# Optimization experiments

Hardware: AMD Instinct MI355X
Metric: run time of the kernel (lower is better)

## Reference

```python
import jax, jax.numpy as jnp
import numpy as np

NUM_NODES = 1024
K = 16384
G = 128

def setup_inputs() -> dict:
    key = jax.random.key(0)
    k1, k2, k3 = jax.random.split(key, 3)
    x = jax.random.normal(k1, (G, NUM_NODES, 64), dtype=jnp.float32)
    # original draws fresh xavier-uniform embeddings inside forward; we
    # materialize equivalent random embeddings here (only ordering matters).
    emb_s = jax.random.normal(k2, (G, NUM_NODES, 1), dtype=jnp.float32)
    emb_t = jax.random.normal(k3, (G, 1, NUM_NODES), dtype=jnp.float32)
    return {"x": x, "emb_s": emb_s, "emb_t": emb_t}

def reference(x, emb_s, emb_t):
    num_graphs = x.shape[0]
    n = NUM_NODES
    # rank-1 outer product adjacency: [G, N, N]
    adj = emb_s * emb_t  # broadcast (G,N,1)*(G,1,N)
    # mask diagonal with -inf
    diag = jnp.eye(n, dtype=bool)
    adj = jnp.where(diag[None, :, :], -jnp.inf, adj)
    # global top-k over flattened N*N per graph
    adj_flat = adj.reshape(num_graphs, n * n)
    _, indices = jax.lax.top_k(adj_flat, K)  # [G, K]
    # scatter ones at selected positions
    out_flat = jnp.zeros((num_graphs, n * n), dtype=adj.dtype)
    rows = jnp.arange(num_graphs)[:, None]
    out_flat = out_flat.at[rows, indices].set(1.0)
    return out_flat.reshape(num_graphs, n, n)
```

## Files before the change

kernel.cpp:

```cpp
#include <hip/hip_runtime.h>
#include <stdint.h>

#define NNODES 1024
#define NGRAPH 128
#define TOPK   16384
#define EQCAP  4096
#define WROWS  8

typedef float vfloat4 __attribute__((ext_vector_type(4)));

__device__ __forceinline__ uint32_t fkey(float x) {
    uint32_t u = __float_as_uint(x);
    return (u & 0x80000000u) ? ~u : (u | 0x80000000u);
}
__device__ __forceinline__ float inv_fkey(uint32_t k) {
    uint32_t u = (k & 0x80000000u) ? (k & 0x7FFFFFFFu) : ~k;
    return __uint_as_float(u);
}

__global__ __launch_bounds__(NNODES)
void select_kernel(const float* __restrict__ s, const float* __restrict__ t,
                   uint32_t* __restrict__ Tout, uint32_t* __restrict__ Rout,
                   uint32_t* __restrict__ eqCntG, uint32_t* __restrict__ eqIdxG) {
    const int g = blockIdx.x, i = threadIdx.x;
    __shared__ uint64_t xbuf[2][NNODES];
    __shared__ float    tvs[NNODES];
    __shared__ uint16_t sidx[NNODES];
    __shared__ uint32_t wsum[16];
    __shared__ uint32_t sLo, sHi, sDir, sEqCnt;
    __shared__ uint32_t sEqList[EQCAP];

    const float tv_i = t[g * NNODES + i];
    uint64_t e = ((uint64_t)fkey(tv_i) << 16) | (uint32_t)i;
    if (i == 0) { sLo = 0u; sHi = 0xFFFFFFFFu; sEqCnt = 0u; }

    int pb = 0;
    for (int k = 2; k <= NNODES; k <<= 1) {
        for (int j = k >> 1; j > 0; j >>= 1) {
            uint64_t pe;
            if (j >= 64) {
                xbuf[pb][i] = e;
                __syncthreads();
                pe = xbuf[pb][i ^ j];
                pb ^= 1;
            } else {
                pe = (uint64_t)__shfl_xor((unsigned long long)e, j, 64);
            }
            bool keepSmall = (((i & j) == 0) == ((i & k) == 0));
            e = (keepSmall == (pe < e)) ? pe : e;
        }
    }
    tvs[i]  = inv_fkey((uint32_t)(e >> 16));
    sidx[i] = (uint16_t)(e & 0xFFFFu);

    const float sv = s[g * NNODES + i];
    const bool sneg = (__float_as_uint(sv) >> 31) != 0;
    const uint32_t kdiag = fkey(sv * tv_i);
    __syncthreads();

    auto srchRange = [&](uint32_t cand, int lo_, int hi_) -> int {
        while (lo_ < hi_) {
            int mid = (lo_ + hi_) >> 1;
            bool pred = fkey(sv * tvs[mid]) > cand;
            bool goLeft = sneg ? !pred : pred;
            if (goLeft) hi_ = mid; else lo_ = mid + 1;
        }
        return lo_;
    };

    int rlo = 0, rhi = NNODES;
    uint32_t cntHi = 0u;

    for (int it = 0; it < 33; ++it) {
        const uint32_t lo = sLo, hi = sHi;
        const uint32_t mid = lo + ((hi - lo) >> 1);
        const int b = srchRange(mid, rlo, rhi);
        uint32_t c = sneg ? (uint32_t)b : (uint32_t)(NNODES - b);
        if (kdiag > mid) c--;
        uint32_t r = c;
        for (int off = 32; off; off >>= 1) r += __shfl_down(r, off);
        if ((i & 63) == 0) wsum[i >> 6] = r;
        __syncthreads();
        if (i == 0 && lo < hi) {
            uint32_t tot = 0;
            for (int w = 0; w < 16; ++w) tot += wsum[w];
            if (tot < TOPK) { sHi = mid; sDir = 0u; cntHi = tot; }
            else            { sLo = mid + 1; sDir = 1u; }
        }
        __syncthreads();
        if (lo < hi) {
            if (sDir == 0u) { if (!sneg) rhi = b; else rlo = b; }
            else            { if (!sneg) rlo = b; else rhi = b; }
        }
    }
    const uint32_t T = sLo;
    if (i == 0) { Tout[g] = T; Rout[g] = TOPK - cntHi; }

    auto bound = [&](bool ge) -> int {
        int lo_ = 0, hi_ = NNODES;
        while (lo_ < hi_) {
            int mid = (lo_ + hi_) >> 1;
            uint32_t k = fkey(sv * tvs[mid]);
            bool pred = ge ? (k >= T) : (k > T);
            bool goLeft = sneg ? !pred : pred;
            if (goLeft) hi_ = mid; else lo_ = mid + 1;
        }
        return lo_;
    };
    int e0, e1;
    if (!sneg) { e0 = bound(true);  e1 = bound(false); }
    else       { e0 = bound(false); e1 = bound(true);  }
    for (int p = e0; p < e1; ++p) {
        uint32_t j = sidx[p];
        if ((int)j == i) continue;
        uint32_t slot = atomicAdd(&sEqCnt, 1u);
        if (slot < EQCAP) sEqList[slot] = (uint32_t)(i * NNODES) + j;
    }
    __syncthreads();
    uint32_t E = sEqCnt; if (E > EQCAP) E = EQCAP;
    if (i == 0) eqCntG[g] = E;
    for (uint32_t p = i; p < E; p += NNODES) eqIdxG[g * EQCAP + p] = sEqList[p];
}

__global__ __launch_bounds__(256)
void write_kernel(const float* __restrict__ s, const float* __restrict__ t,
                  const uint32_t* __restrict__ Tin, float* __restrict__ out) {
    const int b  = blockIdx.x;
    const int g  = b >> 7;
    const int i0 = (b & 127) * WROWS;
    const uint32_t T = Tin[g];
    const vfloat4 tv = ((const vfloat4*)(t + (size_t)g * NNODES))[threadIdx.x];
    const int j0 = threadIdx.x * 4;
    vfloat4* obase = (vfloat4*)(out + (size_t)g * NNODES * NNODES + (size_t)i0 * NNODES);
    #pragma unroll
    for (int r = 0; r < WROWS; ++r) {
        const int i = i0 + r;
        const float sv = s[(size_t)g * NNODES + i];
        vfloat4 o;
        o.x = (fkey(sv * tv.x) > T && (j0 + 0) != i) ? 1.0f : 0.0f;
        o.y = (fkey(sv * tv.y) > T && (j0 + 1) != i) ? 1.0f : 0.0f;
        o.z = (fkey(sv * tv.z) > T && (j0 + 2) != i) ? 1.0f : 0.0f;
        o.w = (fkey(sv * tv.w) > T && (j0 + 3) != i) ? 1.0f : 0.0f;
        __builtin_nontemporal_store(o, &obase[(size_t)r * (NNODES / 4) + threadIdx.x]);
    }
}

__global__ __launch_bounds__(256)
void scatter_kernel(const uint32_t* __restrict__ eqCnt, const uint32_t* __restrict__ eqIdx,
                    const uint32_t* __restrict__ Rin, float* __restrict__ out) {
    const int g = blockIdx.x;
    uint32_t E = eqCnt[g];
    const uint32_t R = Rin[g];
    __shared__ uint32_t se[EQCAP];
    for (uint32_t p = threadIdx.x; p < E; p += blockDim.x) se[p] = eqIdx[g * EQCAP + p];
    __syncthreads();
    for (uint32_t p = threadIdx.x; p < E; p += blockDim.x) {
        uint32_t v = se[p], rank = 0;
        for (uint32_t q = 0; q < E; ++q) rank += (se[q] < v) ? 1u : 0u;
        if (rank < R) out[(size_t)g * NNODES * NNODES + v] = 1.0f;
    }
}

extern "C" void kernel_launch(void* const* d_in, const int* in_sizes, int n_in,
                              void* d_out, int out_size, void* d_ws, size_t ws_size,
                              hipStream_t stream) {
    const float* s = (const float*)d_in[1];
    const float* t = (const float*)d_in[2];
    float* out = (float*)d_out;

    char* ws = (char*)d_ws;
    uint32_t* Tbuf  = (uint32_t*)ws; ws += (size_t)NGRAPH * 4;
    uint32_t* Rbuf  = (uint32_t*)ws; ws += (size_t)NGRAPH * 4;
    uint32_t* eqCnt = (uint32_t*)ws; ws += (size_t)NGRAPH * 4;
    uint32_t* eqIdx = (uint32_t*)ws; ws += (size_t)NGRAPH * EQCAP * 4;

    select_kernel<<<NGRAPH, NNODES, 0, stream>>>(s, t, Tbuf, Rbuf, eqCnt, eqIdx);
    write_kernel<<<NGRAPH * (NNODES / WROWS), 256, 0, stream>>>(s, t, Tbuf, out);
    scatter_kernel<<<NGRAPH, 256, 0, stream>>>(eqCnt, eqIdx, Rbuf, out);
}
```

Measured before the change: 148.2 us.

## Fuse tie scatter into write kernel and use shared-memory bitonic sort

The select kernel's bitonic sort moves from register shuffles plus a double-buffered exchange to an in-place shared-memory compare-swap, with a barrier at every step. The separate scatter kernel is removed: the write kernel now resolves ties at the threshold inline by ranking the element against the equal-key list. The write kernel also becomes a grid-stride loop with 2048 blocks that recomputes indices per float4 and drops nontemporal stores. This saves one launch but adds per-element index math and barriers in the sort, and warps that hit a tie pay a serial rank loop.

```diff
diff --git a/kernel.cpp b/kernel.cpp
--- a/kernel.cpp
+++ b/kernel.cpp
@@ -5,7 +5,6 @@
 #define NGRAPH 128
 #define TOPK   16384
 #define EQCAP  4096
-#define WROWS  8
 
 typedef float vfloat4 __attribute__((ext_vector_type(4)));
 
@@ -13,45 +12,42 @@
     uint32_t u = __float_as_uint(x);
     return (u & 0x80000000u) ? ~u : (u | 0x80000000u);
 }
-__device__ __forceinline__ float inv_fkey(uint32_t k) {
-    uint32_t u = (k & 0x80000000u) ? (k & 0x7FFFFFFFu) : ~k;
-    return __uint_as_float(u);
-}
 
 __global__ __launch_bounds__(NNODES)
 void select_kernel(const float* __restrict__ s, const float* __restrict__ t,
                    uint32_t* __restrict__ Tout, uint32_t* __restrict__ Rout,
                    uint32_t* __restrict__ eqCntG, uint32_t* __restrict__ eqIdxG) {
     const int g = blockIdx.x, i = threadIdx.x;
-    __shared__ uint64_t xbuf[2][NNODES];
+    __shared__ float    torig[NNODES];
+    __shared__ uint32_t skey[NNODES];
+    __shared__ uint16_t sidx[NNODES];
     __shared__ float    tvs[NNODES];
-    __shared__ uint16_t sidx[NNODES];
     __shared__ uint32_t wsum[16];
     __shared__ uint32_t sLo, sHi, sDir, sEqCnt;
     __shared__ uint32_t sEqList[EQCAP];
 
     const float tv_i = t[g * NNODES + i];
-    uint64_t e = ((uint64_t)fkey(tv_i) << 16) | (uint32_t)i;
+    torig[i] = tv_i;
+    skey[i]  = fkey(tv_i);
+    sidx[i]  = (uint16_t)i;
     if (i == 0) { sLo = 0u; sHi = 0xFFFFFFFFu; sEqCnt = 0u; }
 
-    int pb = 0;
     for (int k = 2; k <= NNODES; k <<= 1) {
         for (int j = k >> 1; j > 0; j >>= 1) {
-            uint64_t pe;
-            if (j >= 64) {
-                xbuf[pb][i] = e;
-                __syncthreads();
-                pe = xbuf[pb][i ^ j];
-                pb ^= 1;
-            } else {
-                pe = (uint64_t)__shfl_xor((unsigned long long)e, j, 64);
+            __syncthreads();
+            int partner = i ^ j;
+            if (partner > i) {
+                bool asc = ((i & k) == 0);
+                uint32_t a = skey[i], b = skey[partner];
+                if ((a > b) == asc) {
+                    skey[i] = b; skey[partner] = a;
+                    uint16_t ia = sidx[i]; sidx[i] = sidx[partner]; sidx[partner] = ia;
+                }
             }
-            bool keepSmall = (((i & j) == 0) == ((i & k) == 0));
-            e = (keepSmall == (pe < e)) ? pe : e;
         }
     }
-    tvs[i]  = inv_fkey((uint32_t)(e >> 16));
-    sidx[i] = (uint16_t)(e & 0xFFFFu);
+    __syncthreads();
+    tvs[i] = torig[sidx[i]];
 
     const float sv = s[g * NNODES + i];
     const bool sneg = (__float_as_uint(sv) >> 31) != 0;
@@ -124,40 +120,44 @@
 
 __global__ __launch_bounds__(256)
 void write_kernel(const float* __restrict__ s, const float* __restrict__ t,
-                  const uint32_t* __restrict__ Tin, float* __restrict__ out) {
-    const int b  = blockIdx.x;
-    const int g  = b >> 7;
-    const int i0 = (b & 127) * WROWS;
-    const uint32_t T = Tin[g];
-    const vfloat4 tv = ((const vfloat4*)(t + (size_t)g * NNODES))[threadIdx.x];
-    const int j0 = threadIdx.x * 4;
-    vfloat4* obase = (vfloat4*)(out + (size_t)g * NNODES * NNODES + (size_t)i0 * NNODES);
-    #pragma unroll
-    for (int r = 0; r < WROWS; ++r) {
-        const int i = i0 + r;
-        const float sv = s[(size_t)g * NNODES + i];
+                  const uint32_t* __restrict__ Tin, const uint32_t* __restrict__ Rin,
+                  const uint32_t* __restrict__ eqCntG, const uint32_t* __restrict__ eqIdxG,
+                  float* __restrict__ out) {
+    const uint32_t stride = gridDim.x * blockDim.x;
+    const uint32_t total  = (uint32_t)NGRAPH * NNODES * (NNODES / 4);
+    for (uint32_t f4 = blockIdx.x * blockDim.x + threadIdx.x; f4 < total; f4 += stride) {
+        const uint32_t g  = f4 >> 18;
+        const uint32_t r  = f4 & 0x3FFFFu;
+        const uint32_t i  = r >> 8;
+        const uint32_t c4 = r & 255u;
+        const uint32_t j0 = c4 << 2;
+        const uint32_t T  = Tin[g];
+        const float sv = s[(g << 10) + i];
+        const vfloat4 tv = ((const vfloat4*)t)[(g << 8) + c4];
+        const uint32_t k0 = fkey(sv * tv.x), k1 = fkey(sv * tv.y);
+        const uint32_t k2 = fkey(sv * tv.z), k3 = fkey(sv * tv.w);
         vfloat4 o;
-        o.x = (fkey(sv * tv.x) > T && (j0 + 0) != i) ? 1.0f : 0.0f;
-        o.y = (fkey(sv * tv.y) > T && (j0 + 1) != i) ? 1.0f : 0.0f;
-        o.z = (fkey(sv * tv.z) > T && (j0 + 2) != i) ? 1.0f : 0.0f;
-        o.w = (fkey(sv * tv.w) > T && (j0 + 3) != i) ? 1.0f : 0.0f;
-        __builtin_nontemporal_store(o, &obase[(size_t)r * (NNODES / 4) + threadIdx.x]);
-    }
-}
-
-__global__ __launch_bounds__(256)
-void scatter_kernel(const uint32_t* __restrict__ eqCnt, const uint32_t* __restrict__ eqIdx,
-                    const uint32_t* __restrict__ Rin, float* __restrict__ out) {
-    const int g = blockIdx.x;
-    uint32_t E = eqCnt[g];
-    const uint32_t R = Rin[g];
-    __shared__ uint32_t se[EQCAP];
-    for (uint32_t p = threadIdx.x; p < E; p += blockDim.x) se[p] = eqIdx[g * EQCAP + p];
-    __syncthreads();
-    for (uint32_t p = threadIdx.x; p < E; p += blockDim.x) {
-        uint32_t v = se[p], rank = 0;
-        for (uint32_t q = 0; q < E; ++q) rank += (se[q] < v) ? 1u : 0u;
-        if (rank < R) out[(size_t)g * NNODES * NNODES + v] = 1.0f;
+        o.x = (k0 > T && (j0 + 0) != i) ? 1.0f : 0.0f;
+        o.y = (k1 > T && (j0 + 1) != i) ? 1.0f : 0.0f;
+        o.z = (k2 > T && (j0 + 2) != i) ? 1.0f : 0.0f;
+        o.w = (k3 > T && (j0 + 3) != i) ? 1.0f : 0.0f;
+        if (k0 == T || k1 == T || k2 == T || k3 == T) {
+            uint32_t E = eqCntG[g]; if (E > EQCAP) E = EQCAP;
+            const uint32_t R = Rin[g];
+            const uint32_t* eq = eqIdxG + (size_t)g * EQCAP;
+            const uint32_t kk[4] = {k0, k1, k2, k3};
+            #pragma unroll
+            for (int q = 0; q < 4; ++q) {
+                const uint32_t j = j0 + q;
+                if (kk[q] == T && j != i) {
+                    const uint32_t f = i * NNODES + j;
+                    uint32_t rank = 0;
+                    for (uint32_t e = 0; e < E; ++e) rank += (eq[e] < f) ? 1u : 0u;
+                    if (rank < R) ((float*)&o)[q] = 1.0f;
+                }
+            }
+        }
+        ((vfloat4*)out)[f4] = o;
     }
 }
 
@@ -175,6 +175,5 @@
     uint32_t* eqIdx = (uint32_t*)ws; ws += (size_t)NGRAPH * EQCAP * 4;
 
     select_kernel<<<NGRAPH, NNODES, 0, stream>>>(s, t, Tbuf, Rbuf, eqCnt, eqIdx);
-    write_kernel<<<NGRAPH * (NNODES / WROWS), 256, 0, stream>>>(s, t, Tbuf, out);
-    scatter_kernel<<<NGRAPH, 256, 0, stream>>>(eqCnt, eqIdx, Rbuf, out);
+    write_kernel<<<2048, 256, 0, stream>>>(s, t, Tbuf, Rbuf, eqCnt, eqIdx, out);
 }
```

New measurement: 163.3 us. 10.2% more time.
